# Performance work log

Measured on AMD Instinct MI355X. Metric: run time of the kernel, lower is better.

## Reference

```python
import jax, jax.numpy as jnp
import numpy as np

EPS = 1e-08  # attention offset, matches module epsilon


def _ln(x, g, b, eps=1e-5):
    m = jnp.mean(x, axis=-1, keepdims=True)
    v = jnp.var(x, axis=-1, keepdims=True)
    return (x - m) * jax.lax.rsqrt(v + eps) * g + b


def setup_inputs() -> dict:
    key = jax.random.key(0)
    ks = jax.random.split(key, 12)
    B, N, D, S, H = 32, 16384, 64, 7, 128
    sc = 1.0 / np.sqrt(D)
    sch = 1.0 / np.sqrt(H)
    return {
        "inputs": jax.random.normal(ks[0], (B, N, D), jnp.float32),
        "ln_in_g": jnp.ones((D,), jnp.float32), "ln_in_b": jnp.zeros((D,), jnp.float32),
        "ln_slots_g": jnp.ones((D,), jnp.float32), "ln_slots_b": jnp.zeros((D,), jnp.float32),
        "ln_mlp_g": jnp.ones((D,), jnp.float32), "ln_mlp_b": jnp.zeros((D,), jnp.float32),
        "Wq": jax.random.normal(ks[1], (D, D), jnp.float32) * sc,
        "Wk": jax.random.normal(ks[2], (D, D), jnp.float32) * sc,
        "Wv": jax.random.normal(ks[3], (D, D), jnp.float32) * sc,
        "slots_mu": jax.random.normal(ks[4], (1, 1, D), jnp.float32),
        "slots_log_sigma": jax.random.normal(ks[5], (1, 1, D), jnp.float32) * 0.1,
        "w_ih": jax.random.normal(ks[6], (3 * D, D), jnp.float32) * sc,
        "w_hh": jax.random.normal(ks[7], (3 * D, D), jnp.float32) * sc,
        "b_ih": jnp.zeros((3 * D,), jnp.float32), "b_hh": jnp.zeros((3 * D,), jnp.float32),
        "mlp_w1": jax.random.normal(ks[8], (H, D), jnp.float32) * sc,
        "mlp_b1": jnp.zeros((H,), jnp.float32),
        "mlp_w2": jax.random.normal(ks[9], (D, H), jnp.float32) * sch,
        "mlp_b2": jnp.zeros((D,), jnp.float32),
        "noise_slots": jax.random.normal(ks[10], (B, S, D), jnp.float32),
        "noise_h": jax.random.normal(ks[11], (B, D), jnp.float32),
        "num_iterations": 3,
    }


def reference(inputs, ln_in_g, ln_in_b, ln_slots_g, ln_slots_b, ln_mlp_g, ln_mlp_b,
              Wq, Wk, Wv, slots_mu, slots_log_sigma, w_ih, w_hh, b_ih, b_hh,
              mlp_w1, mlp_b1, mlp_w2, mlp_b2, noise_slots, noise_h, num_iterations):
    D = inputs.shape[-1]
    scale = D ** -0.5

    x = _ln(inputs, ln_in_g, ln_in_b)               # [B,N,D]
    k = jnp.einsum('bnd,ed->bne', x, Wk)            # [B,N,D]
    v = jnp.einsum('bnd,ed->bne', x, Wv)            # [B,N,D]

    sigma = jnp.exp(slots_log_sigma)
    slots = slots_mu + sigma * noise_slots          # [B,S,D]
    h0 = (slots_mu + sigma * noise_h[None])[0]      # [B,D] (torch h0 is [1,B,D])

    def gru_step(h, x_t):  # torch GRU cell, gate order r,z,n
        gi = x_t @ w_ih.T + b_ih
        gh = h @ w_hh.T + b_hh
        ir, iz, inn = jnp.split(gi, 3, axis=-1)
        hr, hz, hn = jnp.split(gh, 3, axis=-1)
        r = jax.nn.sigmoid(ir + hr)
        z = jax.nn.sigmoid(iz + hz)
        n = jnp.tanh(inn + r * hn)
        h_new = (1.0 - z) * n + z * h
        return h_new, h_new

    for _ in range(num_iterations):
        sn = _ln(slots, ln_slots_g, ln_slots_b)
        q = jnp.einsum('bsd,ed->bse', sn, Wq) * scale        # [B,S,D]
        logits = jnp.einsum('bnd,bsd->bns', k, q)            # [B,N,S]
        attn = jax.nn.softmax(logits, axis=-1) + EPS          # softmax over slots
        attn = attn / jnp.sum(attn, axis=1, keepdims=True)   # normalize over inputs (dim=-2)
        updates = jnp.einsum('bns,bnd->bsd', attn, v)        # [B,S,D]
        # nn.GRU over the slot axis as "time", fixed h0 each iteration
        _, hs = jax.lax.scan(gru_step, h0, jnp.swapaxes(updates, 0, 1))
        slots = jnp.swapaxes(hs, 0, 1)                       # [B,S,D]
        hid = jax.nn.relu(_ln(slots, ln_mlp_g, ln_mlp_b) @ mlp_w1.T + mlp_b1)
        slots = slots + (hid @ mlp_w2.T + mlp_b2)
    return slots
```

## Files before the change

kernel.cpp:

```cpp
#include <hip/hip_runtime.h>
#include <hip/hip_bf16.h>


#define B_ 32
#define N_ 16384
#define D_ 64
#define S_ 7

typedef __bf16 bf16x8 __attribute__((ext_vector_type(8)));
typedef float floatx4 __attribute__((ext_vector_type(4)));

__device__ __forceinline__ unsigned int f2bfu(float f) {
  __hip_bfloat16 h = __float2bfloat16(f);
  return (unsigned int)__builtin_bit_cast(unsigned short, h);
}
__device__ __forceinline__ unsigned int pack2bf(float lo, float hi) {
  return f2bfu(lo) | (f2bfu(hi) << 16);
}

__device__ void q_from_slots(const float* s_slot, float* s_tmp,
                             const float* __restrict__ g, const float* __restrict__ bb,
                             const float* __restrict__ Wq, float* __restrict__ qout,
                             int lane, int w)
{
  for (int ss = 0; ss < 2; ++ss) {
    int srow = ss * 4 + w;
    if (srow < 7) {
      float xv = s_slot[srow * 64 + lane];
      float s1 = xv, s2 = xv * xv;
#pragma unroll
      for (int mm = 1; mm < 64; mm <<= 1) {
        s1 += __shfl_xor(s1, mm);
        s2 += __shfl_xor(s2, mm);
      }
      float mean = s1 * 0.015625f;
      float var = s2 * 0.015625f - mean * mean;
      float rs = rsqrtf(var + 1e-5f);
      s_tmp[w * 64 + lane] = (xv - mean) * rs * g[lane] + bb[lane];
    }
    __syncthreads();
    if (srow < 7) {
      float acc = 0.f;
      const float4* wr = (const float4*)(Wq + lane * 64);
      const float4* xr = (const float4*)(s_tmp + w * 64);
#pragma unroll
      for (int i = 0; i < 16; ++i) {
        float4 a = wr[i], xx = xr[i];
        acc += a.x * xx.x + a.y * xx.y + a.z * xx.z + a.w * xx.w;
      }
      qout[srow * 64 + lane] = acc * 0.125f;
    }
    __syncthreads();
  }
}

__global__ __launch_bounds__(256) void init_kernel(
    const float* __restrict__ mu, const float* __restrict__ lsig,
    const float* __restrict__ nslots, const float* __restrict__ nh,
    const float* __restrict__ ln_s_g, const float* __restrict__ ln_s_b,
    const float* __restrict__ Wq,
    const float* __restrict__ Wk, const float* __restrict__ Wv,
    float* __restrict__ qbuf, float* __restrict__ h0b,
    unsigned short* __restrict__ wkb, unsigned short* __restrict__ wvb)
{
  __shared__ float s_slot[448];
  __shared__ float s_tmp[256];
  const int b = blockIdx.x, t = threadIdx.x, lane = t & 63, w = t >> 6;
  {
    int gid = b * 256 + t;
    if (gid < 4096) wkb[gid] = (unsigned short)f2bfu(Wk[gid]);
    else            wvb[gid - 4096] = (unsigned short)f2bfu(Wv[gid - 4096]);
  }
  for (int o = t; o < 448; o += 256) {
    int d = o & 63;
    s_slot[o] = mu[d] + expf(lsig[d]) * nslots[b * 448 + o];
  }
  if (t < 64) h0b[b * 64 + t] = mu[t] + expf(lsig[t]) * nh[b * 64 + t];
  __syncthreads();
  q_from_slots(s_slot, s_tmp, ln_s_g, ln_s_b, Wq, qbuf + b * 448, lane, w);
}

__global__ __launch_bounds__(256, 4) void proj_kernel(
    const float* __restrict__ x,
    const float* __restrict__ lng, const float* __restrict__ lnb,
    const unsigned short* __restrict__ wkb, const unsigned short* __restrict__ wvb,
    const float* __restrict__ qbuf,
    unsigned short* __restrict__ kb, unsigned short* __restrict__ vt,
    float* __restrict__ Wp, float* __restrict__ Cp)
{
  __shared__ __align__(16) unsigned char smemA[18432];
  __shared__ __align__(16) unsigned short s_vo[64 * 136];
  __shared__ __align__(16) unsigned short s_qb[1024];
  __shared__ float s_cred[4][8];
  unsigned short* s_xn = (unsigned short*)smemA;
  unsigned short* s_ko = (unsigned short*)smemA;
  unsigned short* s_at = (unsigned short*)smemA;
  float* s_red = (float*)(smemA + 5120);

  const int t = threadIdx.x, lane = t & 63, w = t >> 6;
  const int R0 = blockIdx.x * 128;
  const int bb = R0 >> 14;
  const int nbase = R0 & (N_ - 1);
  const int chunk = nbase >> 7;

  {
    int i0 = t * 4;
    int s = i0 >> 6, d0 = i0 & 63;
    float f0 = 0.f, f1 = 0.f, f2 = 0.f, f3 = 0.f;
    if (s < 7) {
      const float* qp = qbuf + bb * 448 + s * 64 + d0;
      f0 = qp[0]; f1 = qp[1]; f2 = qp[2]; f3 = qp[3];
    }
    uint2 p;
    p.x = pack2bf(f0, f1);
    p.y = pack2bf(f2, f3);
    *(uint2*)&s_qb[i0] = p;
  }

  const int ql = t & 3;
  float4 g4[4], b4[4];
#pragma unroll
  for (int j = 0; j < 4; ++j) {
    g4[j] = *(const float4*)&lng[ql * 16 + j * 4];
    b4[j] = *(const float4*)&lnb[ql * 16 + j * 4];
  }
#pragma unroll
  for (int half = 0; half < 2; ++half) {
    int r = half * 64 + (t >> 2);
    const float4* xp = (const float4*)&x[(size_t)(R0 + r) * 64 + ql * 16];
    float4 xv[4];
#pragma unroll
    for (int j = 0; j < 4; ++j) xv[j] = xp[j];
    float s1 = 0.f, s2 = 0.f;
#pragma unroll
    for (int j = 0; j < 4; ++j) {
      s1 += xv[j].x + xv[j].y + xv[j].z + xv[j].w;
      s2 += xv[j].x * xv[j].x + xv[j].y * xv[j].y + xv[j].z * xv[j].z + xv[j].w * xv[j].w;
    }
    s1 += __shfl_xor(s1, 1); s2 += __shfl_xor(s2, 1);
    s1 += __shfl_xor(s1, 2); s2 += __shfl_xor(s2, 2);
    float mean = s1 * 0.015625f;
    float var = s2 * 0.015625f - mean * mean;
    float rs = rsqrtf(var + 1e-5f);
    float y[16];
#pragma unroll
    for (int j = 0; j < 4; ++j) {
      y[j * 4 + 0] = (xv[j].x - mean) * rs * g4[j].x + b4[j].x;
      y[j * 4 + 1] = (xv[j].y - mean) * rs * g4[j].y + b4[j].y;
      y[j * 4 + 2] = (xv[j].z - mean) * rs * g4[j].z + b4[j].z;
      y[j * 4 + 3] = (xv[j].w - mean) * rs * g4[j].w + b4[j].w;
    }
#pragma unroll
    for (int h = 0; h < 2; ++h) {
      uint4 p;
      p.x = pack2bf(y[h * 8 + 0], y[h * 8 + 1]);
      p.y = pack2bf(y[h * 8 + 2], y[h * 8 + 3]);
      p.z = pack2bf(y[h * 8 + 4], y[h * 8 + 5]);
      p.w = pack2bf(y[h * 8 + 6], y[h * 8 + 7]);
      int c = ql * 2 + h;
      int sc = c ^ (r & 7);
      *(uint4*)&s_xn[r * 64 + sc * 8] = p;
    }
  }
  __syncthreads();

  const int m16 = lane & 15, quad = lane >> 4;
  bf16x8 bq0 = *(const bf16x8*)&s_qb[m16 * 64 + quad * 8];
  bf16x8 bq1 = *(const bf16x8*)&s_qb[m16 * 64 + 32 + quad * 8];

  bf16x8 bf[2][2];
#pragma unroll
  for (int rt = 0; rt < 2; ++rt) {
    int xr = (w * 2 + rt) * 16 + m16;
#pragma unroll
    for (int kk = 0; kk < 2; ++kk)
      bf[rt][kk] = *(const bf16x8*)&s_xn[xr * 64 + (((kk * 4 + quad) ^ (xr & 7)) * 8)];
  }
  bf16x8 wkf[4][2], wvf[4][2];
#pragma unroll
  for (int ft = 0; ft < 4; ++ft)
#pragma unroll
    for (int kk = 0; kk < 2; ++kk) {
      wkf[ft][kk] = *(const bf16x8*)&wkb[(ft * 16 + m16) * 64 + kk * 32 + quad * 8];
      wvf[ft][kk] = *(const bf16x8*)&wvb[(ft * 16 + m16) * 64 + kk * 32 + quad * 8];
    }
  __syncthreads();

#pragma unroll
  for (int ft = 0; ft < 4; ++ft)
#pragma unroll
    for (int rt = 0; rt < 2; ++rt) {
      floatx4 acc = (floatx4){0.f, 0.f, 0.f, 0.f};
      acc = __builtin_amdgcn_mfma_f32_16x16x32_bf16(wkf[ft][0], bf[rt][0], acc, 0, 0, 0);
      acc = __builtin_amdgcn_mfma_f32_16x16x32_bf16(wkf[ft][1], bf[rt][1], acc, 0, 0, 0);
      int n_l = (w * 2 + rt) * 16 + m16;
      uint2 p;
      p.x = pack2bf(acc[0], acc[1]);
      p.y = pack2bf(acc[2], acc[3]);
      *(uint2*)&s_ko[n_l * 72 + ft * 16 + quad * 4] = p;
    }
  __syncthreads();

#pragma unroll
  for (int ft = 0; ft < 4; ++ft)
#pragma unroll
    for (int rt = 0; rt < 2; ++rt) {
      floatx4 acc = (floatx4){0.f, 0.f, 0.f, 0.f};
      acc = __builtin_amdgcn_mfma_f32_16x16x32_bf16(bf[rt][0], wvf[ft][0], acc, 0, 0, 0);
      acc = __builtin_amdgcn_mfma_f32_16x16x32_bf16(bf[rt][1], wvf[ft][1], acc, 0, 0, 0);
      int n_l = (w * 2 + rt) * 16 + quad * 4;
      int d0 = ft * 16 + m16;
      uint2 p;
      p.x = pack2bf(acc[0], acc[1]);
      p.y = pack2bf(acc[2], acc[3]);
      *(uint2*)&s_vo[d0 * 136 + n_l] = p;
    }
  bf16x8 ak[2][2];
#pragma unroll
  for (int rt = 0; rt < 2; ++rt) {
    int row = (w * 2 + rt) * 16 + m16;
    ak[rt][0] = *(const bf16x8*)&s_ko[row * 72 + quad * 8];
    ak[rt][1] = *(const bf16x8*)&s_ko[row * 72 + 32 + quad * 8];
  }
#pragma unroll
  for (int p = 0; p < 4; ++p) {
    int ii = (p * 256 + t) * 8;
    int n_l = ii >> 6, dl = ii & 63;
    uint4 v4 = *(const uint4*)&s_ko[n_l * 72 + dl];
    *(uint4*)&kb[(size_t)(R0 + n_l) * 64 + dl] = v4;
  }
  __syncthreads();

  float cl = 0.f;
#pragma unroll
  for (int rt = 0; rt < 2; ++rt) {
    floatx4 c = (floatx4){0.f, 0.f, 0.f, 0.f};
    c = __builtin_amdgcn_mfma_f32_16x16x32_bf16(ak[rt][0], bq0, c, 0, 0, 0);
    c = __builtin_amdgcn_mfma_f32_16x16x32_bf16(ak[rt][1], bq1, c, 0, 0, 0);
    float atv[4];
#pragma unroll
    for (int rg = 0; rg < 4; ++rg) {
      float e = (m16 < 7) ? __expf(c[rg]) : 0.f;
      float sm = e;
      sm += __shfl_xor(sm, 1);
      sm += __shfl_xor(sm, 2);
      sm += __shfl_xor(sm, 4);
      float a = e * __builtin_amdgcn_rcpf(sm) + 1e-8f;
      atv[rg] = a;
      cl += a;
    }
    if (m16 < 7) {
      uint2 p;
      p.x = pack2bf(atv[0], atv[1]);
      p.y = pack2bf(atv[2], atv[3]);
      *(uint2*)&s_at[w * 640 + m16 * 40 + rt * 16 + quad * 4] = p;
    }
  }
  asm volatile("s_waitcnt lgkmcnt(0)" ::: "memory");
  bf16x8 af = *(const bf16x8*)&s_at[w * 640 + m16 * 40 + quad * 8];
  floatx4 acc2[4];
#pragma unroll
  for (int dt = 0; dt < 4; ++dt) acc2[dt] = (floatx4){0.f, 0.f, 0.f, 0.f};
#pragma unroll
  for (int dt = 0; dt < 4; ++dt) {
    bf16x8 bv = *(const bf16x8*)&s_vo[(dt * 16 + m16) * 136 + w * 32 + quad * 8];
    acc2[dt] = __builtin_amdgcn_mfma_f32_16x16x32_bf16(af, bv, acc2[dt], 0, 0, 0);
  }
  if (quad < 2) {
#pragma unroll
    for (int dt = 0; dt < 4; ++dt)
#pragma unroll
      for (int rg = 0; rg < 4; ++rg) {
        int s = quad * 4 + rg;
        if (s < 7) s_red[w * 448 + s * 64 + dt * 16 + m16] = acc2[dt][rg];
      }
  }
  cl += __shfl_xor(cl, 16);
  cl += __shfl_xor(cl, 32);
  if (m16 < 7 && quad == 0) s_cred[w][m16] = cl;
  __syncthreads();

  for (int o = t; o < 448; o += 256) {
    float v = s_red[o] + s_red[448 + o] + s_red[896 + o] + s_red[1344 + o];
    Wp[((size_t)bb * 128 + chunk) * 448 + o] = v;
  }
  if (t < 7) {
    float c = s_cred[0][t] + s_cred[1][t] + s_cred[2][t] + s_cred[3][t];
    Cp[((size_t)bb * 128 + chunk) * 8 + t] = c;
  }
#pragma unroll
  for (int p = 0; p < 4; ++p) {
    int ii = (p * 256 + t) * 8;
    int d0 = ii >> 7, nl = ii & 127;
    uint4 v4 = *(const uint4*)&s_vo[d0 * 136 + nl];
    *(uint4*)&vt[((size_t)bb * 64 + d0) * N_ + nbase + nl] = v4;
  }
}

__global__ __launch_bounds__(512, 4) void attn_kernel(
    const unsigned short* __restrict__ kb, const unsigned short* __restrict__ vt,
    const float* __restrict__ qbuf,
    float* __restrict__ Wp, float* __restrict__ Cp)
{
  __shared__ __align__(16) unsigned short s_qb[16 * 64];
  __shared__ __align__(16) unsigned short s_at[8][16 * 72];
  __shared__ __align__(16) float s_red[8][448];
  __shared__ float s_cred[8][8];

  const int b = blockIdx.y;
  const int t = threadIdx.x, lane = t & 63, w = t >> 6;
  const int m16 = lane & 15, quad = lane >> 4;

  if (t < 256) {
    int i0 = t * 4;
    int s = i0 >> 6, d0 = i0 & 63;
    float f0 = 0.f, f1 = 0.f, f2 = 0.f, f3 = 0.f;
    if (s < 7) {
      const float* qp = qbuf + b * 448 + s * 64 + d0;
      f0 = qp[0]; f1 = qp[1]; f2 = qp[2]; f3 = qp[3];
    }
    uint2 p;
    p.x = pack2bf(f0, f1);
    p.y = pack2bf(f2, f3);
    *(uint2*)&s_qb[i0] = p;
  }
  __syncthreads();

  bf16x8 bq0 = *(const bf16x8*)&s_qb[m16 * 64 + quad * 8];
  bf16x8 bq1 = *(const bf16x8*)&s_qb[m16 * 64 + 32 + quad * 8];

  const int n0w = blockIdx.x * 512 + w * 64;
  const unsigned short* kbA = kb + ((size_t)b * N_ + n0w) * 64;

  bf16x8 ak[4][2];
#pragma unroll
  for (int nt = 0; nt < 4; ++nt) {
    ak[nt][0] = *(const bf16x8*)&kbA[(size_t)(nt * 16 + m16) * 64 + quad * 8];
    ak[nt][1] = *(const bf16x8*)&kbA[(size_t)(nt * 16 + m16) * 64 + 32 + quad * 8];
  }
  floatx4 cc[4];
#pragma unroll
  for (int nt = 0; nt < 4; ++nt) {
    floatx4 c = (floatx4){0.f, 0.f, 0.f, 0.f};
    c = __builtin_amdgcn_mfma_f32_16x16x32_bf16(ak[nt][0], bq0, c, 0, 0, 0);
    c = __builtin_amdgcn_mfma_f32_16x16x32_bf16(ak[nt][1], bq1, c, 0, 0, 0);
    cc[nt] = c;
  }
  float cl = 0.f;
#pragma unroll
  for (int nt = 0; nt < 4; ++nt) {
    float atv[4];
#pragma unroll
    for (int rg = 0; rg < 4; ++rg) {
      float e = (m16 < 7) ? __expf(cc[nt][rg]) : 0.f;
      float sm = e;
      sm += __shfl_xor(sm, 1);
      sm += __shfl_xor(sm, 2);
      sm += __shfl_xor(sm, 4);
      float a = e * __builtin_amdgcn_rcpf(sm) + 1e-8f;
      atv[rg] = a;
      cl += a;
    }
    if (m16 < 7) {
      uint2 p;
      p.x = pack2bf(atv[0], atv[1]);
      p.y = pack2bf(atv[2], atv[3]);
      *(uint2*)&s_at[w][m16 * 72 + nt * 16 + quad * 4] = p;
    }
  }

  bf16x8 bv[2][4];
  const unsigned short* vtB = vt + (size_t)b * 64 * N_ + n0w;
#pragma unroll
  for (int ch = 0; ch < 2; ++ch)
#pragma unroll
    for (int dt = 0; dt < 4; ++dt)
      bv[ch][dt] = *(const bf16x8*)&vtB[(size_t)(dt * 16 + m16) * N_ + ch * 32 + quad * 8];
  asm volatile("s_waitcnt lgkmcnt(0)" ::: "memory");
  bf16x8 af0 = *(const bf16x8*)&s_at[w][m16 * 72 + quad * 8];
  bf16x8 af1 = *(const bf16x8*)&s_at[w][m16 * 72 + 32 + quad * 8];

  floatx4 acc[4];
#pragma unroll
  for (int dt = 0; dt < 4; ++dt) acc[dt] = (floatx4){0.f, 0.f, 0.f, 0.f};
#pragma unroll
  for (int dt = 0; dt < 4; ++dt)
    acc[dt] = __builtin_amdgcn_mfma_f32_16x16x32_bf16(af0, bv[0][dt], acc[dt], 0, 0, 0);
#pragma unroll
  for (int dt = 0; dt < 4; ++dt)
    acc[dt] = __builtin_amdgcn_mfma_f32_16x16x32_bf16(af1, bv[1][dt], acc[dt], 0, 0, 0);

  if (quad < 2) {
#pragma unroll
    for (int dt = 0; dt < 4; ++dt)
#pragma unroll
      for (int rg = 0; rg < 4; ++rg) {
        int s = quad * 4 + rg;
        if (s < 7) s_red[w][s * 64 + dt * 16 + m16] = acc[dt][rg];
      }
  }
  cl += __shfl_xor(cl, 16);
  cl += __shfl_xor(cl, 32);
  if (m16 < 7 && quad == 0) s_cred[w][m16] = cl;
  __syncthreads();

  if (t < 448) {
    float v = 0.f;
#pragma unroll
    for (int wv = 0; wv < 8; ++wv) v += s_red[wv][t];
    Wp[((size_t)b * 32 + blockIdx.x) * 448 + t] = v;
  } else if (t < 455) {
    int s = t - 448;
    float c = 0.f;
#pragma unroll
    for (int wv = 0; wv < 8; ++wv) c += s_cred[wv][s];
    Cp[((size_t)b * 32 + blockIdx.x) * 8 + s] = c;
  }
}

__global__ __launch_bounds__(512) void slot_update_kernel(
    const float* __restrict__ Wp, const float* __restrict__ Cp, int npart,
    const float* __restrict__ h0b,
    const float* __restrict__ w_ih, const float* __restrict__ w_hh,
    const float* __restrict__ b_ih, const float* __restrict__ b_hh,
    const float* __restrict__ ln_m_g, const float* __restrict__ ln_m_b,
    const float* __restrict__ w1, const float* __restrict__ b1,
    const float* __restrict__ w2, const float* __restrict__ b2,
    const float* __restrict__ ln_s_g, const float* __restrict__ ln_s_b,
    const float* __restrict__ Wq,
    float* __restrict__ qbuf, float* __restrict__ out, int flags)
{
  const int b = blockIdx.x, t = threadIdx.x, lane = t & 63, w = t >> 6;
  __shared__ float s_whhT[64 * 201];
  __shared__ float s_upd[448];
  __shared__ float s_gi[1344];
  __shared__ float s_h[64];
  __shared__ float s_gh[192];
  __shared__ float s_slot[448];
  __shared__ float s_tmp[512];
  __shared__ float s_cs[8];

  for (int i = t; i < 12288; i += 512) {
    int j = i >> 6, d = i & 63;
    s_whhT[d * 201 + j] = w_hh[i];
  }
  if (t < 7) {
    float cs = 0.f;
#pragma unroll 8
    for (int p = 0; p < npart; ++p) cs += Cp[((size_t)b * npart + p) * 8 + t];
    s_cs[t] = cs;
  }
  if (t < 64) s_h[t] = h0b[b * 64 + t];
  __syncthreads();
  if (t < 448) {
    float acc = 0.f;
#pragma unroll 8
    for (int p = 0; p < npart; ++p) acc += Wp[((size_t)b * npart + p) * 448 + t];
    s_upd[t] = acc / s_cs[t >> 6];
  }
  __syncthreads();
  for (int o = t; o < 1344; o += 512) {
    int s = o / 192, j = o - s * 192;
    float acc = b_ih[j];
    const float4* wr = (const float4*)(w_ih + j * 64);
    const float4* ur = (const float4*)(s_upd + s * 64);
#pragma unroll
    for (int i = 0; i < 16; ++i) {
      float4 a = wr[i], u = ur[i];
      acc += a.x * u.x + a.y * u.y + a.z * u.z + a.w * u.w;
    }
    s_gi[o] = acc;
  }
  __syncthreads();
  for (int s = 0; s < 7; ++s) {
    if (t < 192) {
      float acc = b_hh[t];
#pragma unroll 16
      for (int d = 0; d < 64; ++d) acc += s_h[d] * s_whhT[d * 201 + t];
      s_gh[t] = acc;
    }
    __syncthreads();
    if (t < 64) {
      float ir = s_gi[s * 192 + t], iz = s_gi[s * 192 + 64 + t], inn = s_gi[s * 192 + 128 + t];
      float hr = s_gh[t], hz = s_gh[64 + t], hn = s_gh[128 + t];
      float r = 1.f / (1.f + expf(-(ir + hr)));
      float z = 1.f / (1.f + expf(-(iz + hz)));
      float n = tanhf(inn + r * hn);
      float hnew = (1.f - z) * n + z * s_h[t];
      s_slot[s * 64 + t] = hnew;
      s_h[t] = hnew;
    }
    __syncthreads();
  }
  float* s_sn = s_gi;
  float* s_hid = s_gi + 448;
  if (w < 7) {
    float xv = s_slot[w * 64 + lane];
    float s1 = xv, s2 = xv * xv;
#pragma unroll
    for (int mm = 1; mm < 64; mm <<= 1) {
      s1 += __shfl_xor(s1, mm);
      s2 += __shfl_xor(s2, mm);
    }
    float mean = s1 * 0.015625f;
    float var = s2 * 0.015625f - mean * mean;
    float rs = rsqrtf(var + 1e-5f);
    s_sn[w * 64 + lane] = (xv - mean) * rs * ln_m_g[lane] + ln_m_b[lane];
  }
  __syncthreads();
  for (int o = t; o < 896; o += 512) {
    int s = o >> 7, hh = o & 127;
    float acc = b1[hh];
    const float4* wr = (const float4*)(w1 + hh * 64);
    const float4* xr = (const float4*)(s_sn + s * 64);
#pragma unroll
    for (int i = 0; i < 16; ++i) {
      float4 a = wr[i], xx = xr[i];
      acc += a.x * xx.x + a.y * xx.y + a.z * xx.z + a.w * xx.w;
    }
    s_hid[o] = fmaxf(acc, 0.f);
  }
  __syncthreads();
  for (int o = t; o < 448; o += 512) {
    int s = o >> 6, d = o & 63;
    float acc = b2[d];
    const float4* wr = (const float4*)(w2 + d * 128);
    const float4* hr = (const float4*)(s_hid + s * 128);
#pragma unroll
    for (int i = 0; i < 32; ++i) {
      float4 a = wr[i], hv = hr[i];
      acc += a.x * hv.x + a.y * hv.y + a.z * hv.z + a.w * hv.w;
    }
    float val = s_slot[o] + acc;
    s_slot[o] = val;
    if (flags & 1) out[b * 448 + o] = val;
  }
  __syncthreads();
  if (flags & 2) {
    if (w < 7) {
      float xv = s_slot[w * 64 + lane];
      float s1 = xv, s2 = xv * xv;
#pragma unroll
      for (int mm = 1; mm < 64; mm <<= 1) {
        s1 += __shfl_xor(s1, mm);
        s2 += __shfl_xor(s2, mm);
      }
      float mean = s1 * 0.015625f;
      float var = s2 * 0.015625f - mean * mean;
      float rs = rsqrtf(var + 1e-5f);
      s_tmp[w * 64 + lane] = (xv - mean) * rs * ln_s_g[lane] + ln_s_b[lane];
    }
    __syncthreads();
    if (w < 7) {
      float acc = 0.f;
      const float4* wr = (const float4*)(Wq + lane * 64);
      const float4* xr = (const float4*)(s_tmp + w * 64);
#pragma unroll
      for (int i = 0; i < 16; ++i) {
        float4 a = wr[i], xx = xr[i];
        acc += a.x * xx.x + a.y * xx.y + a.z * xx.z + a.w * xx.w;
      }
      qbuf[b * 448 + w * 64 + lane] = acc * 0.125f;
    }
  }
}

extern "C" void kernel_launch(void* const* d_in, const int* in_sizes, int n_in,
                              void* d_out, int out_size, void* d_ws, size_t ws_size,
                              hipStream_t stream)
{
  (void)in_sizes; (void)n_in; (void)out_size; (void)ws_size;
  const float* x      = (const float*)d_in[0];
  const float* ln_in_g = (const float*)d_in[1];
  const float* ln_in_b = (const float*)d_in[2];
  const float* ln_s_g  = (const float*)d_in[3];
  const float* ln_s_b  = (const float*)d_in[4];
  const float* ln_m_g  = (const float*)d_in[5];
  const float* ln_m_b  = (const float*)d_in[6];
  const float* Wq = (const float*)d_in[7];
  const float* Wk = (const float*)d_in[8];
  const float* Wv = (const float*)d_in[9];
  const float* mu = (const float*)d_in[10];
  const float* lsig = (const float*)d_in[11];
  const float* w_ih = (const float*)d_in[12];
  const float* w_hh = (const float*)d_in[13];
  const float* b_ih = (const float*)d_in[14];
  const float* b_hh = (const float*)d_in[15];
  const float* w1 = (const float*)d_in[16];
  const float* b1 = (const float*)d_in[17];
  const float* w2 = (const float*)d_in[18];
  const float* b2 = (const float*)d_in[19];
  const float* nslots = (const float*)d_in[20];
  const float* nh = (const float*)d_in[21];

  unsigned short* kb  = (unsigned short*)d_ws;
  unsigned short* vt  = kb + (size_t)B_ * N_ * D_;
  unsigned short* wkb = vt + (size_t)B_ * N_ * D_;
  unsigned short* wvb = wkb + 4096;
  float* fb  = (float*)(wvb + 4096);
  float* qbuf = fb;
  float* h0b  = fb + 14336;
  float* Wp   = fb + 16384;
  float* Cp   = Wp + 1835008;
  float* out = (float*)d_out;

  init_kernel<<<32, 256, 0, stream>>>(mu, lsig, nslots, nh, ln_s_g, ln_s_b, Wq,
                                      Wk, Wv, qbuf, h0b, wkb, wvb);
  proj_kernel<<<4096, 256, 0, stream>>>(x, ln_in_g, ln_in_b, wkb, wvb, qbuf, kb, vt, Wp, Cp);
  slot_update_kernel<<<32, 512, 0, stream>>>(Wp, Cp, 128, h0b, w_ih, w_hh, b_ih, b_hh,
                                             ln_m_g, ln_m_b, w1, b1, w2, b2,
                                             ln_s_g, ln_s_b, Wq, qbuf, out, 2);
  attn_kernel<<<dim3(32, 32), 512, 0, stream>>>(kb, vt, qbuf, Wp, Cp);
  slot_update_kernel<<<32, 512, 0, stream>>>(Wp, Cp, 32, h0b, w_ih, w_hh, b_ih, b_hh,
                                             ln_m_g, ln_m_b, w1, b1, w2, b2,
                                             ln_s_g, ln_s_b, Wq, qbuf, out, 2);
  attn_kernel<<<dim3(32, 32), 512, 0, stream>>>(kb, vt, qbuf, Wp, Cp);
  slot_update_kernel<<<32, 512, 0, stream>>>(Wp, Cp, 32, h0b, w_ih, w_hh, b_ih, b_hh,
                                             ln_m_g, ln_m_b, w1, b1, w2, b2,
                                             ln_s_g, ln_s_b, Wq, qbuf, out, 1);
}
```

Measured before the change: 427.0 us.

## Tile V^T layout per 128-row chunk, shrink attn blocks, run GRU recurrence in one wavefront

The transposed V buffer moves from a [B][D][N] layout to per-128-row tiles of [D][128], so each projection block writes a contiguous 16KB tile and each attention wave reads V from a compact region instead of 64 rows strided by N. The attention kernel drops from 512 to 256 threads per block and doubles the grid, and the slot update now sums 64 partials instead of 32. The GRU recurrence in the slot update runs in a single wavefront, broadcasting the hidden state with shuffles instead of going through shared memory, which removes two block-wide barriers per step. This trades some parallelism in the hidden-to-hidden matvec for lower barrier latency on a serial path.

```diff
diff --git a/kernel.cpp b/kernel.cpp
--- a/kernel.cpp
+++ b/kernel.cpp
@@ -100,8 +100,7 @@
   const int t = threadIdx.x, lane = t & 63, w = t >> 6;
   const int R0 = blockIdx.x * 128;
   const int bb = R0 >> 14;
-  const int nbase = R0 & (N_ - 1);
-  const int chunk = nbase >> 7;
+  const int tile = blockIdx.x;
 
   {
     int i0 = t * 4;
@@ -282,36 +281,36 @@
 
   for (int o = t; o < 448; o += 256) {
     float v = s_red[o] + s_red[448 + o] + s_red[896 + o] + s_red[1344 + o];
-    Wp[((size_t)bb * 128 + chunk) * 448 + o] = v;
+    Wp[(size_t)tile * 448 + o] = v;
   }
   if (t < 7) {
     float c = s_cred[0][t] + s_cred[1][t] + s_cred[2][t] + s_cred[3][t];
-    Cp[((size_t)bb * 128 + chunk) * 8 + t] = c;
+    Cp[(size_t)tile * 8 + t] = c;
   }
 #pragma unroll
   for (int p = 0; p < 4; ++p) {
     int ii = (p * 256 + t) * 8;
     int d0 = ii >> 7, nl = ii & 127;
     uint4 v4 = *(const uint4*)&s_vo[d0 * 136 + nl];
-    *(uint4*)&vt[((size_t)bb * 64 + d0) * N_ + nbase + nl] = v4;
-  }
-}
-
-__global__ __launch_bounds__(512, 4) void attn_kernel(
+    *(uint4*)&vt[(size_t)tile * 8192 + ii] = v4;
+  }
+}
+
+__global__ __launch_bounds__(256, 4) void attn_kernel(
     const unsigned short* __restrict__ kb, const unsigned short* __restrict__ vt,
     const float* __restrict__ qbuf,
     float* __restrict__ Wp, float* __restrict__ Cp)
 {
   __shared__ __align__(16) unsigned short s_qb[16 * 64];
-  __shared__ __align__(16) unsigned short s_at[8][16 * 72];
-  __shared__ __align__(16) float s_red[8][448];
-  __shared__ float s_cred[8][8];
+  __shared__ __align__(16) unsigned short s_at[4][16 * 72];
+  __shared__ __align__(16) float s_red[4][448];
+  __shared__ float s_cred[4][8];
 
   const int b = blockIdx.y;
   const int t = threadIdx.x, lane = t & 63, w = t >> 6;
   const int m16 = lane & 15, quad = lane >> 4;
 
-  if (t < 256) {
+  {
     int i0 = t * 4;
     int s = i0 >> 6, d0 = i0 & 63;
     float f0 = 0.f, f1 = 0.f, f2 = 0.f, f3 = 0.f;
@@ -329,7 +328,7 @@
   bf16x8 bq0 = *(const bf16x8*)&s_qb[m16 * 64 + quad * 8];
   bf16x8 bq1 = *(const bf16x8*)&s_qb[m16 * 64 + 32 + quad * 8];
 
-  const int n0w = blockIdx.x * 512 + w * 64;
+  const int n0w = blockIdx.x * 256 + w * 64;
   const unsigned short* kbA = kb + ((size_t)b * N_ + n0w) * 64;
 
   bf16x8 ak[4][2];
@@ -370,12 +369,12 @@
   }
 
   bf16x8 bv[2][4];
-  const unsigned short* vtB = vt + (size_t)b * 64 * N_ + n0w;
+  const unsigned short* vtB = vt + (size_t)(b * 128 + (n0w >> 7)) * 8192 + (n0w & 127);
 #pragma unroll
   for (int ch = 0; ch < 2; ++ch)
 #pragma unroll
     for (int dt = 0; dt < 4; ++dt)
-      bv[ch][dt] = *(const bf16x8*)&vtB[(size_t)(dt * 16 + m16) * N_ + ch * 32 + quad * 8];
+      bv[ch][dt] = *(const bf16x8*)&vtB[(dt * 16 + m16) * 128 + ch * 32 + quad * 8];
   asm volatile("s_waitcnt lgkmcnt(0)" ::: "memory");
   bf16x8 af0 = *(const bf16x8*)&s_at[w][m16 * 72 + quad * 8];
   bf16x8 af1 = *(const bf16x8*)&s_at[w][m16 * 72 + 32 + quad * 8];
@@ -404,17 +403,13 @@
   if (m16 < 7 && quad == 0) s_cred[w][m16] = cl;
   __syncthreads();
 
-  if (t < 448) {
-    float v = 0.f;
-#pragma unroll
-    for (int wv = 0; wv < 8; ++wv) v += s_red[wv][t];
-    Wp[((size_t)b * 32 + blockIdx.x) * 448 + t] = v;
-  } else if (t < 455) {
-    int s = t - 448;
-    float c = 0.f;
-#pragma unroll
-    for (int wv = 0; wv < 8; ++wv) c += s_cred[wv][s];
-    Cp[((size_t)b * 32 + blockIdx.x) * 8 + s] = c;
+  for (int o = t; o < 448; o += 256) {
+    float v = s_red[0][o] + s_red[1][o] + s_red[2][o] + s_red[3][o];
+    Wp[((size_t)b * 64 + blockIdx.x) * 448 + o] = v;
+  }
+  if (t < 7) {
+    float c = s_cred[0][t] + s_cred[1][t] + s_cred[2][t] + s_cred[3][t];
+    Cp[((size_t)b * 64 + blockIdx.x) * 8 + t] = c;
   }
 }
 
@@ -434,8 +429,6 @@
   __shared__ float s_whhT[64 * 201];
   __shared__ float s_upd[448];
   __shared__ float s_gi[1344];
-  __shared__ float s_h[64];
-  __shared__ float s_gh[192];
   __shared__ float s_slot[448];
   __shared__ float s_tmp[512];
   __shared__ float s_cs[8];
@@ -450,7 +443,6 @@
     for (int p = 0; p < npart; ++p) cs += Cp[((size_t)b * npart + p) * 8 + t];
     s_cs[t] = cs;
   }
-  if (t < 64) s_h[t] = h0b[b * 64 + t];
   __syncthreads();
   if (t < 448) {
     float acc = 0.f;
@@ -472,26 +464,30 @@
     s_gi[o] = acc;
   }
   __syncthreads();
-  for (int s = 0; s < 7; ++s) {
-    if (t < 192) {
-      float acc = b_hh[t];
-#pragma unroll 16
-      for (int d = 0; d < 64; ++d) acc += s_h[d] * s_whhT[d * 201 + t];
-      s_gh[t] = acc;
-    }
-    __syncthreads();
-    if (t < 64) {
-      float ir = s_gi[s * 192 + t], iz = s_gi[s * 192 + 64 + t], inn = s_gi[s * 192 + 128 + t];
-      float hr = s_gh[t], hz = s_gh[64 + t], hn = s_gh[128 + t];
-      float r = 1.f / (1.f + expf(-(ir + hr)));
-      float z = 1.f / (1.f + expf(-(iz + hz)));
-      float n = tanhf(inn + r * hn);
-      float hnew = (1.f - z) * n + z * s_h[t];
-      s_slot[s * 64 + t] = hnew;
-      s_h[t] = hnew;
-    }
-    __syncthreads();
-  }
+  if (w == 0) {
+    float h = h0b[b * 64 + lane];
+    const float bhr = b_hh[lane], bhz = b_hh[64 + lane], bhn = b_hh[128 + lane];
+    const float* wr_ = &s_whhT[lane];
+    const float* wz_ = &s_whhT[64 + lane];
+    const float* wn_ = &s_whhT[128 + lane];
+    for (int s = 0; s < 7; ++s) {
+      float ar = bhr, az = bhz, an = bhn;
+#pragma unroll 8
+      for (int d = 0; d < 64; ++d) {
+        float hd = __shfl(h, d);
+        ar += hd * wr_[d * 201];
+        az += hd * wz_[d * 201];
+        an += hd * wn_[d * 201];
+      }
+      float ir = s_gi[s * 192 + lane], iz = s_gi[s * 192 + 64 + lane], inn = s_gi[s * 192 + 128 + lane];
+      float r = 1.f / (1.f + __expf(-(ir + ar)));
+      float z = 1.f / (1.f + __expf(-(iz + az)));
+      float n = tanhf(inn + r * an);
+      h = (1.f - z) * n + z * h;
+      s_slot[s * 64 + lane] = h;
+    }
+  }
+  __syncthreads();
   float* s_sn = s_gi;
   float* s_hid = s_gi + 448;
   if (w < 7) {
@@ -610,12 +606,12 @@
   slot_update_kernel<<<32, 512, 0, stream>>>(Wp, Cp, 128, h0b, w_ih, w_hh, b_ih, b_hh,
                                              ln_m_g, ln_m_b, w1, b1, w2, b2,
                                              ln_s_g, ln_s_b, Wq, qbuf, out, 2);
-  attn_kernel<<<dim3(32, 32), 512, 0, stream>>>(kb, vt, qbuf, Wp, Cp);
-  slot_update_kernel<<<32, 512, 0, stream>>>(Wp, Cp, 32, h0b, w_ih, w_hh, b_ih, b_hh,
+  attn_kernel<<<dim3(64, 32), 256, 0, stream>>>(kb, vt, qbuf, Wp, Cp);
+  slot_update_kernel<<<32, 512, 0, stream>>>(Wp, Cp, 64, h0b, w_ih, w_hh, b_ih, b_hh,
                                              ln_m_g, ln_m_b, w1, b1, w2, b2,
                                              ln_s_g, ln_s_b, Wq, qbuf, out, 2);
-  attn_kernel<<<dim3(32, 32), 512, 0, stream>>>(kb, vt, qbuf, Wp, Cp);
-  slot_update_kernel<<<32, 512, 0, stream>>>(Wp, Cp, 32, h0b, w_ih, w_hh, b_ih, b_hh,
+  attn_kernel<<<dim3(64, 32), 256, 0, stream>>>(kb, vt, qbuf, Wp, Cp);
+  slot_update_kernel<<<32, 512, 0, stream>>>(Wp, Cp, 64, h0b, w_ih, w_hh, b_ih, b_hh,
                                              ln_m_g, ln_m_b, w1, b1, w2, b2,
                                              ln_s_g, ln_s_b, Wq, qbuf, out, 1);
 }
```

After: 449.5 us. 1.05x slower.
